# Optimization experiments

Hardware: AMD Instinct MI355X
Metric: run time of the kernel (lower is better)

The kernel has to match this reference:

```python
import jax, jax.numpy as jnp
import numpy as np

H = 16  # n_heads (init kwarg)


def pos_enc(length, dim):
    # torch PositionalEncoding: pe[:,0::2]=sin, pe[:,1::2]=cos
    pos = jnp.arange(length, dtype=jnp.float32)[:, None]
    div = jnp.exp(jnp.arange(0, dim, 2, dtype=jnp.float32) * (-np.log(10000.0) / dim))
    ang = pos * div  # [L, dim/2]
    return jnp.stack([jnp.sin(ang), jnp.cos(ang)], axis=-1).reshape(length, dim)


def torch_ln(x, a, b, eps=1e-6):
    # custom LayerNorm: a*(x-mean)/(std+eps)+b with unbiased std (torch default)
    mean = x.mean(-1, keepdims=True)
    n = x.shape[-1]
    var = ((x - mean) ** 2).sum(-1, keepdims=True) / (n - 1)
    return a * (x - mean) / (jnp.sqrt(var) + eps) + b


def setup_inputs() -> dict:
    key = jax.random.key(0)
    ks = jax.random.split(key, 16)
    B, Lq, Lk, qd, kd, hid, mid = 8, 512, 1024, 768, 768, 1024, 4096
    s = 0.02  # weight init scale
    w = lambda k, shape: jax.random.normal(k, shape, jnp.float32) * s
    return dict(
        q=jax.random.normal(ks[0], (B, Lq, qd), jnp.float32),
        k=jax.random.normal(ks[1], (B, Lk, kd), jnp.float32),
        Wq=w(ks[2], (qd, hid)), bq=jnp.zeros(hid, jnp.float32),
        Wk=w(ks[3], (kd, hid)), bk=jnp.zeros(hid, jnp.float32),
        Wv=w(ks[4], (kd, hid)), bv=jnp.zeros(hid, jnp.float32),
        Wv0=w(ks[5], (kd, hid)), bv0=jnp.zeros(hid, jnp.float32),
        Wq0=w(ks[6], (qd, hid)), bq0=jnp.zeros(hid, jnp.float32),
        nq_a=jnp.ones(hid, jnp.float32), nq_b=jnp.zeros(hid, jnp.float32),
        nx_a=jnp.ones(hid, jnp.float32), nx_b=jnp.zeros(hid, jnp.float32),
        W1=w(ks[7], (hid, mid)), b1=jnp.zeros(mid, jnp.float32),
        W2=w(ks[8], (mid, hid)), b2=jnp.zeros(hid, jnp.float32),
        ns_a=jnp.ones(hid, jnp.float32), ns_b=jnp.zeros(hid, jnp.float32),
    )


def reference(q, k, Wq, bq, Wk, bk, Wv, bv, Wv0, bv0, Wq0, bq0,
              nq_a, nq_b, nx_a, nx_b, W1, b1, W2, b2, ns_a, ns_b):
    # FocalAtt(mode='CA').forward(q, k, PE='qk', SF=True, outmode='atted_bilinear')
    B, Lq, qd = q.shape
    Lk, kd = k.shape[1], k.shape[2]
    hid = Wq.shape[1]
    dh = hid // H
    q0 = q
    qp = q + pos_enc(Lq, qd)  # PosEnc_q (dropout=0)
    kp = k + pos_enc(Lk, kd)  # PosEnc_k
    # AttM: manual multi-head scores
    qh = (qp @ Wq + bq).reshape(B, Lq, H, dh).transpose(0, 2, 1, 3)  # bhqd
    kh = (kp @ Wk + bk).reshape(B, Lk, H, dh).transpose(0, 2, 1, 3)  # bhkd
    scores = jnp.einsum('bhqd,bhkd->bhqk', qh, kh) / jnp.sqrt(jnp.float32(dh))
    att = jax.nn.softmax(scores, axis=-1)  # SF=True
    q0p = q0 @ Wq0 + bq0  # [B, Lq, hid]
    # 'atted' branch
    v1 = (kp @ Wv + bv).reshape(B, Lk, H, dh).transpose(0, 2, 1, 3)
    atted = jnp.einsum('bhqk,bhkd->bhqd', att, v1)
    atted = atted.transpose(0, 2, 1, 3).reshape(B, Lq, hid)
    atted = torch_ln(q0p + atted, nq_a, nq_b)
    # 'bilinear' branch: einsum('bhvk,bhvq,bhqk->bhk')
    q0h = q0p.reshape(B, Lq, H, dh).transpose(0, 2, 1, 3)  # bhvd, v=Lq
    v0 = (kp @ Wv0 + bv0).reshape(B, Lk, H, dh).transpose(0, 2, 1, 3)  # bhqd, q=Lk
    x = jnp.einsum('bhvd,bhvq,bhqd->bhd', q0h, att, v0).reshape(B, hid)
    x = torch_ln(x, nx_a, nx_b)
    # attention output: relu over scores, mean over heads
    att_out = jax.nn.relu(scores).sum(axis=1) / jnp.float32(H)  # [B, Lq, Lk]
    # SorCA: FFN + residual + LayerNorm
    ff = jax.nn.relu(atted @ W1 + b1) @ W2 + b2
    qq = torch_ln(atted + ff, ns_a, ns_b)
    # FocalAtt returns (feature, q, k, attention, attidx_q, attidx_k); drop Nones
    return (x, qq, kp, att_out)
```

## Files before the change

kernel.cpp:

```cpp
#include <hip/hip_runtime.h>


typedef unsigned short bfr;
using short8 = __attribute__((ext_vector_type(8))) short;
using f32x4  = __attribute__((ext_vector_type(4))) float;

__device__ __forceinline__ float b2f(bfr s) {
  return __uint_as_float(((unsigned int)s) << 16);
}
__device__ __forceinline__ bfr f2b(float f) {
  unsigned int u = __float_as_uint(f);
  u += 0x7fffu + ((u >> 16) & 1u);
  return (bfr)(u >> 16);
}

struct __align__(8) us4 { bfr x, y, z, w; };

__device__ __forceinline__ float4 load4f(const float* p) { return *(const float4*)p; }
__device__ __forceinline__ float4 load4f(const bfr* p) {
  us4 u = *(const us4*)p;
  return make_float4(b2f(u.x), b2f(u.y), b2f(u.z), b2f(u.w));
}
__device__ __forceinline__ void store4(float* p, float a, float b, float c, float d) {
  *(float4*)p = make_float4(a, b, c, d);
}
__device__ __forceinline__ void store4(bfr* p, float a, float b, float c, float d) {
  us4 v; v.x = f2b(a); v.y = f2b(b); v.z = f2b(c); v.w = f2b(d);
  *(us4*)p = v;
}

__device__ __forceinline__ void gll16(const bfr* g, bfr* l) {
  __builtin_amdgcn_global_load_lds(
      (const __attribute__((address_space(1))) unsigned int*)g,
      (__attribute__((address_space(3))) unsigned int*)l, 16, 0, 0);
}

__device__ __forceinline__ int swz_off(int row, int chunk) {
  return row * 64 + ((chunk ^ (row & 7)) * 8);
}

__device__ __forceinline__ float pe_val(int l, int d) {
  float ang = (float)l * expf((float)(d & ~1) * (-9.210340371976184f / 768.0f));
  return (d & 1) ? cosf(ang) : sinf(ang);
}

__global__ __launch_bounds__(256) void posenc_k(const float* __restrict__ in,
                                                float* __restrict__ outf,
                                                bfr* __restrict__ outb, int total) {
  int idx = blockIdx.x * 256 + threadIdx.x;
  if (idx >= total) return;
  float v = in[idx] + pe_val((idx / 768) % 1024, idx % 768);
  outf[idx] = v;
  outb[idx] = f2b(v);
}

__global__ __launch_bounds__(256) void posenc_q_all(const float* __restrict__ in,
                                                    bfr* __restrict__ out,
                                                    bfr* __restrict__ outraw,
                                                    int total) {
  int idx = blockIdx.x * 256 + threadIdx.x;
  if (idx >= total) return;
  float v = in[idx];
  out[idx] = f2b(v + pe_val((idx / 768) % 512, idx % 768));
  outraw[idx] = f2b(v);
}

__global__ __launch_bounds__(256) void transpose_w(const float* __restrict__ src,
                                                   bfr* __restrict__ dst,
                                                   int rows, int cols, int ld,
                                                   int mode) {
  __shared__ float t[32][33];
  const int bc = blockIdx.x * 32, br = blockIdx.y * 32;
  const int tx = threadIdx.x & 31, ty = threadIdx.x >> 5;
#pragma unroll
  for (int i = 0; i < 4; i++)
    t[ty + i * 8][tx] = src[(size_t)(br + ty + i * 8) * ld + bc + tx];
  __syncthreads();
#pragma unroll
  for (int i = 0; i < 4; i++) {
    int c = bc + ty + i * 8;
    int r = (mode == 0) ? c : ((c >> 6) * 128 + (c & 63) + (mode == 2 ? 64 : 0));
    dst[(size_t)r * rows + br + tx] = f2b(t[tx][ty + i * 8]);
  }
}

template <typename TC>
__device__ __forceinline__ void mgemm_body64(const bfr* __restrict__ A,
                                             const bfr* __restrict__ BT,
                                             const float* __restrict__ bias,
                                             TC* __restrict__ C,
                                             int K, int ldc, int relu, int accum,
                                             int m0, int n0,
                                             bfr* __restrict__ As,
                                             bfr* __restrict__ Bs) {
  const int tid = threadIdx.x;
  const int lane = tid & 63, w = tid >> 6;
  const int wm = (w & 1) * 64, wn = (w >> 1) * 32;
  const int grow = lane >> 3;
  const int gkc = ((lane & 7) ^ (lane >> 3)) * 8;
  const int fr = lane & 15, fcg = lane >> 4;
  const int NT = K >> 6;
  f32x4 acc[4][2];
#pragma unroll
  for (int i = 0; i < 4; i++)
#pragma unroll
    for (int j = 0; j < 2; j++) acc[i][j] = (f32x4){0.f, 0.f, 0.f, 0.f};

  auto issue = [&](int t, int buf) {
    const int k0 = t << 6;
    const bfr* Ag = A + (size_t)(m0 + w * 32 + grow) * K + k0 + gkc;
#pragma unroll
    for (int i = 0; i < 4; i++)
      gll16(Ag + (size_t)(i * 8) * K, As + buf * 8192 + (w * 32 + i * 8) * 64);
    const bfr* Bg = BT + (size_t)(n0 + w * 16 + grow) * K + k0 + gkc;
#pragma unroll
    for (int i = 0; i < 2; i++)
      gll16(Bg + (size_t)(i * 8) * K, Bs + buf * 4096 + (w * 16 + i * 8) * 64);
  };

  issue(0, 0);
  asm volatile("s_waitcnt vmcnt(0)" ::: "memory");
  __builtin_amdgcn_s_barrier();
  __builtin_amdgcn_sched_barrier(0);
  int cur = 0;
  for (int t = 0; t < NT; ++t) {
    const bool more = (t + 1 < NT);
    if (more) issue(t + 1, cur ^ 1);
    __builtin_amdgcn_s_setprio(1);
#pragma unroll
    for (int ks = 0; ks < 2; ks++) {
      short8 af[4], bf4[2];
#pragma unroll
      for (int i = 0; i < 4; i++)
        af[i] = *(const short8*)(As + cur * 8192 + swz_off(wm + i * 16 + fr, ks * 4 + fcg));
#pragma unroll
      for (int j = 0; j < 2; j++)
        bf4[j] = *(const short8*)(Bs + cur * 4096 + swz_off(wn + j * 16 + fr, ks * 4 + fcg));
#pragma unroll
      for (int i = 0; i < 4; i++)
#pragma unroll
        for (int j = 0; j < 2; j++)
          acc[i][j] = __builtin_amdgcn_mfma_f32_16x16x32_bf16(af[i], bf4[j], acc[i][j], 0, 0, 0);
    }
    __builtin_amdgcn_s_setprio(0);
    if (more) {
      asm volatile("s_waitcnt vmcnt(0)" ::: "memory");
      __builtin_amdgcn_s_barrier();
      __builtin_amdgcn_sched_barrier(0);
      cur ^= 1;
    }
  }
  const int col0 = n0 + wn + fr;
  const int row0 = m0 + wm + (lane >> 4) * 4;
  float bsv[2];
#pragma unroll
  for (int j = 0; j < 2; j++) bsv[j] = bias ? bias[col0 + j * 16] : 0.f;
#pragma unroll
  for (int i = 0; i < 4; i++) {
#pragma unroll
    for (int j = 0; j < 2; j++) {
      const int col = col0 + j * 16;
#pragma unroll
      for (int r = 0; r < 4; r++) {
        const int row = row0 + i * 16 + r;
        float v = acc[i][j][r] + bsv[j];
        if (relu) v = fmaxf(v, 0.f);
        size_t idx = (size_t)row * ldc + col;
        if constexpr (sizeof(TC) == 2) {
          C[idx] = f2b(v);
        } else {
          if (accum) C[idx] += v; else C[idx] = v;
        }
      }
    }
  }
}

template <typename TC>
__global__ __launch_bounds__(256) void mgemm64(const bfr* __restrict__ A,
                                               const bfr* __restrict__ BT,
                                               const float* __restrict__ bias,
                                               TC* __restrict__ C,
                                               int K, int ldc, int relu, int accum) {
  __shared__ bfr As[2][8192];
  __shared__ bfr Bs[2][4096];
  const int nwg = gridDim.x * gridDim.y;
  const int bid = blockIdx.y * gridDim.x + blockIdx.x;
  const int q8 = nwg >> 3, r8 = nwg & 7;
  const int xcd = bid & 7, off = bid >> 3;
  const int swz = (xcd < r8 ? xcd * (q8 + 1) : r8 * (q8 + 1) + (xcd - r8) * q8) + off;
  const int n0 = (swz % gridDim.x) * 64, m0 = (swz / gridDim.x) * 128;
  mgemm_body64<TC>(A, BT, bias, C, K, ldc, relu, accum, m0, n0,
                   &As[0][0], &Bs[0][0]);
}

__global__ __launch_bounds__(256) void kv_gemm2(const bfr* __restrict__ kp0,
                                                const bfr* __restrict__ kp1,
                                                const bfr* __restrict__ WkT,
                                                const float* __restrict__ bk,
                                                bfr* __restrict__ kh0,
                                                bfr* __restrict__ kh1,
                                                const bfr* __restrict__ WTvv,
                                                bfr* __restrict__ vT0,
                                                bfr* __restrict__ vT1) {
  __shared__ bfr As[2][8192];
  __shared__ bfr Bs[2][4096];
  const int swz = (blockIdx.x & 7) * 96 + (blockIdx.x >> 3);
  if (swz < 128) {
    mgemm_body64<bfr>(kp0, WkT, bk, kh0, 768, 1024, 0, 0,
                      (swz >> 4) * 128, (swz & 15) * 64, &As[0][0], &Bs[0][0]);
  } else if (swz < 256) {
    const int s = swz - 128;
    mgemm_body64<bfr>(kp1, WkT, bk, kh1, 768, 1024, 0, 0,
                      (s >> 4) * 128, (s & 15) * 64, &As[0][0], &Bs[0][0]);
  } else if (swz < 512) {
    const int s = swz - 256;
    mgemm_body64<bfr>(WTvv, kp0, nullptr, vT0, 768, 1024, 0, 0,
                      (s >> 4) * 128, (s & 15) * 64, &As[0][0], &Bs[0][0]);
  } else {
    const int s = swz - 512;
    mgemm_body64<bfr>(WTvv, kp1, nullptr, vT1, 768, 1024, 0, 0,
                      (s >> 4) * 128, (s & 15) * 64, &As[0][0], &Bs[0][0]);
  }
}

__global__ __launch_bounds__(256) void proj_gemm(const bfr* __restrict__ q16,
                                                 const bfr* __restrict__ Wq0T,
                                                 const float* __restrict__ bq0,
                                                 bfr* __restrict__ q0p,
                                                 const bfr* __restrict__ qp_all,
                                                 const bfr* __restrict__ WqT,
                                                 const float* __restrict__ bq,
                                                 bfr* __restrict__ qh) {
  __shared__ bfr As[2][8192];
  __shared__ bfr Bs[2][4096];
  const int swz = (blockIdx.x & 7) * 128 + (blockIdx.x >> 3);
  if (swz < 512) {
    mgemm_body64<bfr>(q16, Wq0T, bq0, q0p, 768, 1024, 0, 0,
                      (swz >> 4) * 128, (swz & 15) * 64, &As[0][0], &Bs[0][0]);
  } else {
    const int s = swz - 512;
    mgemm_body64<bfr>(qp_all, WqT, bq, qh, 768, 1024, 0, 0,
                      (s >> 4) * 128, (s & 15) * 64, &As[0][0], &Bs[0][0]);
  }
}

__global__ __launch_bounds__(256) void score_mfma(const bfr* __restrict__ qh,
                                                  const bfr* __restrict__ kh,
                                                  bfr* __restrict__ sc) {
  __shared__ __align__(16) bfr Qs[128][72];
  __shared__ __align__(16) bfr Ks[128][72];
  const int h = blockIdx.z, q0 = blockIdx.y * 128, k0 = blockIdx.x * 128;
  const int tid = threadIdx.x, lane = tid & 63;
  const int wm = ((tid >> 6) & 1) * 64, wn = (tid >> 7) * 64;
  const int fr = lane & 15, fc = (lane >> 4) * 8;
  {
    const int r = tid >> 1, c = (tid & 1) * 32;
    const bfr* qsrc = qh + (size_t)(q0 + r) * 1024 + h * 64 + c;
    const bfr* ksrc = kh + (size_t)(k0 + r) * 1024 + h * 64 + c;
#pragma unroll
    for (int i = 0; i < 4; i++) {
      *(short8*)&Qs[r][c + i * 8] = *(const short8*)(qsrc + i * 8);
      *(short8*)&Ks[r][c + i * 8] = *(const short8*)(ksrc + i * 8);
    }
  }
  __syncthreads();
  f32x4 acc[4][4];
#pragma unroll
  for (int i = 0; i < 4; i++)
#pragma unroll
    for (int j = 0; j < 4; j++) acc[i][j] = (f32x4){0.f, 0.f, 0.f, 0.f};
  __builtin_amdgcn_s_setprio(1);
#pragma unroll
  for (int ks = 0; ks < 2; ks++) {
    short8 af[4], bf[4];
#pragma unroll
    for (int t = 0; t < 4; t++) af[t] = *(const short8*)&Qs[wm + t * 16 + fr][ks * 32 + fc];
#pragma unroll
    for (int t = 0; t < 4; t++) bf[t] = *(const short8*)&Ks[wn + t * 16 + fr][ks * 32 + fc];
#pragma unroll
    for (int i = 0; i < 4; i++)
#pragma unroll
      for (int j = 0; j < 4; j++)
        acc[i][j] = __builtin_amdgcn_mfma_f32_16x16x32_bf16(af[i], bf[j], acc[i][j], 0, 0, 0);
  }
  __builtin_amdgcn_s_setprio(0);
  const int col0 = k0 + wn + fr;
  const int row0 = q0 + wm + (lane >> 4) * 4;
#pragma unroll
  for (int i = 0; i < 4; i++)
#pragma unroll
    for (int j = 0; j < 4; j++)
#pragma unroll
      for (int r = 0; r < 4; r++)
        sc[((size_t)h * 512 + row0 + i * 16 + r) * 1024 + col0 + j * 16] =
            f2b(acc[i][j][r] * 0.125f);
}

__global__ __launch_bounds__(256) void smax_ao(bfr* __restrict__ sc,
                                               float* __restrict__ ao) {
  __shared__ float part[4][1024];
  const int q = blockIdx.x;
  const int tid = threadIdx.x, lane = tid & 63, w = tid >> 6;
  float aos[16];
#pragma unroll
  for (int i = 0; i < 16; i++) aos[i] = 0.f;
#pragma unroll
  for (int i = 0; i < 4; i++) {
    const int h = w * 4 + i;
    bfr* row = sc + ((size_t)h * 512 + q) * 1024 + lane * 16;
    us4 raw[4];
    float v[16];
#pragma unroll
    for (int j = 0; j < 4; j++) raw[j] = ((const us4*)row)[j];
#pragma unroll
    for (int j = 0; j < 4; j++) {
      v[j * 4 + 0] = b2f(raw[j].x); v[j * 4 + 1] = b2f(raw[j].y);
      v[j * 4 + 2] = b2f(raw[j].z); v[j * 4 + 3] = b2f(raw[j].w);
    }
    float m = v[0];
#pragma unroll
    for (int j = 1; j < 16; j++) m = fmaxf(m, v[j]);
#pragma unroll
    for (int j = 0; j < 16; j++) aos[j] += fmaxf(v[j], 0.f);
    for (int o = 32; o; o >>= 1) m = fmaxf(m, __shfl_xor(m, o, 64));
    float s = 0.f;
#pragma unroll
    for (int j = 0; j < 16; j++) { v[j] = expf(v[j] - m); s += v[j]; }
    for (int o = 32; o; o >>= 1) s += __shfl_xor(s, o, 64);
    const float inv = 1.0f / s;
#pragma unroll
    for (int j = 0; j < 4; j++) {
      raw[j].x = f2b(v[j * 4 + 0] * inv); raw[j].y = f2b(v[j * 4 + 1] * inv);
      raw[j].z = f2b(v[j * 4 + 2] * inv); raw[j].w = f2b(v[j * 4 + 3] * inv);
      ((us4*)row)[j] = raw[j];
    }
  }
#pragma unroll
  for (int j = 0; j < 4; j++)
    *(float4*)&part[w][lane * 16 + j * 4] =
        make_float4(aos[j * 4], aos[j * 4 + 1], aos[j * 4 + 2], aos[j * 4 + 3]);
  __syncthreads();
  const int k4 = tid * 4;
  float4 a0 = *(const float4*)&part[0][k4];
  float4 a1 = *(const float4*)&part[1][k4];
  float4 a2 = *(const float4*)&part[2][k4];
  float4 a3 = *(const float4*)&part[3][k4];
  store4(ao + (size_t)q * 1024 + k4,
         (a0.x + a1.x + a2.x + a3.x) * 0.0625f, (a0.y + a1.y + a2.y + a3.y) * 0.0625f,
         (a0.z + a1.z + a2.z + a3.z) * 0.0625f, (a0.w + a1.w + a2.w + a3.w) * 0.0625f);
}

__global__ __launch_bounds__(256) void attv3(const bfr* __restrict__ att,
                                             const bfr* __restrict__ vT,
                                             const float* __restrict__ bv,
                                             const float* __restrict__ bv0,
                                             bfr* __restrict__ atp,
                                             bfr* __restrict__ u) {
  __shared__ bfr As[2][16 * 64];
  __shared__ bfr Bs[2][128 * 64];
  const int h = blockIdx.y, q0 = blockIdx.x * 16;
  const int tid = threadIdx.x, lane = tid & 63, w = tid >> 6;
  const int fr = lane & 15, fcg = lane >> 4;
  const int wn = w * 32;
  const bfr* attb = att + ((size_t)h * 512 + q0) * 1024;
  const bfr* vb = vT + (size_t)h * 128 * 1024;
  const int grow = lane >> 3;
  const int gkc = ((lane & 7) ^ (lane >> 3)) * 8;
  f32x4 acc[2];
#pragma unroll
  for (int j = 0; j < 2; j++) acc[j] = (f32x4){0.f, 0.f, 0.f, 0.f};

  auto issue = [&](int t, int buf) {
    const int k0 = t << 6;
    if (w < 2)
      gll16(attb + (size_t)(w * 8 + grow) * 1024 + k0 + gkc, &As[buf][(w * 8) * 64]);
#pragma unroll
    for (int i = 0; i < 4; i++)
      gll16(vb + (size_t)(wn + i * 8 + grow) * 1024 + k0 + gkc,
            &Bs[buf][(wn + i * 8) * 64]);
  };

  issue(0, 0);
  asm volatile("s_waitcnt vmcnt(0)" ::: "memory");
  __builtin_amdgcn_s_barrier();
  __builtin_amdgcn_sched_barrier(0);
  int cur = 0;
  for (int t = 0; t < 16; ++t) {
    const bool more = (t + 1 < 16);
    if (more) issue(t + 1, cur ^ 1);
    __builtin_amdgcn_s_setprio(1);
#pragma unroll
    for (int ks = 0; ks < 2; ks++) {
      short8 af = *(const short8*)&As[cur][swz_off(fr, ks * 4 + fcg)];
#pragma unroll
      for (int j = 0; j < 2; j++) {
        short8 bf = *(const short8*)&Bs[cur][swz_off(wn + j * 16 + fr, ks * 4 + fcg)];
        acc[j] = __builtin_amdgcn_mfma_f32_16x16x32_bf16(af, bf, acc[j], 0, 0, 0);
      }
    }
    __builtin_amdgcn_s_setprio(0);
    if (more) {
      asm volatile("s_waitcnt vmcnt(0)" ::: "memory");
      __builtin_amdgcn_s_barrier();
      __builtin_amdgcn_sched_barrier(0);
      cur ^= 1;
    }
  }
  const int row0 = q0 + (lane >> 4) * 4;
  bfr* o = (w < 2) ? atp : u;
  const float* bias = (w < 2) ? bv : bv0;
  const int dbase = wn & 63;
#pragma unroll
  for (int j = 0; j < 2; j++) {
    const int cm = dbase + j * 16 + fr;
    const float bb = bias[h * 64 + cm];
#pragma unroll
    for (int r = 0; r < 4; r++)
      o[(size_t)(row0 + r) * 1024 + h * 64 + cm] = f2b(acc[j][r] + bb);
  }
}

__global__ __launch_bounds__(256) void xpre2(const bfr* __restrict__ q0p0,
                                             const bfr* __restrict__ u0,
                                             float* __restrict__ xpre0) {
  const int c = blockIdx.x * 256 + threadIdx.x;
  const int r0 = blockIdx.y * 64;
  const int j = blockIdx.z;
  const bfr* qp = q0p0 + (size_t)j * 524288 + (size_t)r0 * 1024 + c;
  const bfr* up = u0 + (size_t)j * 1048576 + (size_t)r0 * 1024 + c;
  float s = 0.f;
#pragma unroll 8
  for (int r = 0; r < 64; r++)
    s = fmaf(b2f(qp[(size_t)r * 1024]), b2f(up[(size_t)r * 1024]), s);
  atomicAdd(&xpre0[j * 1024 + c], s);
}

template <typename OT>
__device__ __forceinline__ void ln_body(float4 v, const float* ga, const float* be,
                                        OT* outp, int tid, float* sm) {
  float s = v.x + v.y + v.z + v.w;
  for (int o = 32; o; o >>= 1) s += __shfl_down(s, o, 64);
  if ((tid & 63) == 0) sm[tid >> 6] = s;
  __syncthreads();
  s = sm[0] + sm[1] + sm[2] + sm[3];
  float mean = s * (1.0f / 1024.0f);
  float d0 = v.x - mean, d1 = v.y - mean, d2 = v.z - mean, d3 = v.w - mean;
  float q = d0 * d0 + d1 * d1 + d2 * d2 + d3 * d3;
  __syncthreads();
  for (int o = 32; o; o >>= 1) q += __shfl_down(q, o, 64);
  if ((tid & 63) == 0) sm[tid >> 6] = q;
  __syncthreads();
  q = sm[0] + sm[1] + sm[2] + sm[3];
  float rs = 1.0f / (sqrtf(q * (1.0f / 1023.0f)) + 1e-6f);
  float4 g = *(const float4*)(ga + tid * 4);
  float4 bb = *(const float4*)(be + tid * 4);
  store4(outp, g.x * d0 * rs + bb.x, g.y * d1 * rs + bb.y,
         g.z * d2 * rs + bb.z, g.w * d3 * rs + bb.w);
}

template <typename TX, typename TY, typename OT>
__global__ __launch_bounds__(256) void ln_kernel(const TX* __restrict__ X,
                                                 const TY* __restrict__ Y,
                                                 const float* __restrict__ ga,
                                                 const float* __restrict__ be,
                                                 OT* __restrict__ out) {
  __shared__ float sm[4];
  const size_t row = blockIdx.x;
  const int tid = threadIdx.x;
  float4 v = load4f(X + row * 1024 + tid * 4);
  if (Y) {
    float4 w = load4f(Y + row * 1024 + tid * 4);
    v.x += w.x; v.y += w.y; v.z += w.z; v.w += w.w;
  }
  ln_body(v, ga, be, out + row * 1024 + tid * 4, tid, sm);
}

__global__ __launch_bounds__(256) void ln2_kernel(const bfr* __restrict__ q0p0,
                                                  const bfr* __restrict__ atp0,
                                                  const float* __restrict__ ga,
                                                  const float* __restrict__ be,
                                                  bfr* __restrict__ atl0) {
  __shared__ float sm[4];
  const int row = blockIdx.x;
  const int b = row >> 9, r = row & 511;
  const int tid = threadIdx.x;
  float4 v = load4f(q0p0 + (size_t)b * 524288 + (size_t)r * 1024 + tid * 4);
  float4 w = load4f(atp0 + (size_t)b * 1048576 + (size_t)r * 1024 + tid * 4);
  v.x += w.x; v.y += w.y; v.z += w.z; v.w += w.w;
  ln_body(v, ga, be, atl0 + (size_t)b * 524288 + (size_t)r * 1024 + tid * 4, tid, sm);
}

extern "C" void kernel_launch(void* const* d_in, const int* in_sizes, int n_in,
                              void* d_out, int out_size, void* d_ws, size_t ws_size,
                              hipStream_t stream) {
  (void)in_sizes; (void)n_in; (void)out_size; (void)ws_size;
  const float* q   = (const float*)d_in[0];
  const float* k   = (const float*)d_in[1];
  const float* Wq  = (const float*)d_in[2];
  const float* bq  = (const float*)d_in[3];
  const float* Wk  = (const float*)d_in[4];
  const float* bk  = (const float*)d_in[5];
  const float* Wv  = (const float*)d_in[6];
  const float* bv  = (const float*)d_in[7];
  const float* Wv0 = (const float*)d_in[8];
  const float* bv0 = (const float*)d_in[9];
  const float* Wq0 = (const float*)d_in[10];
  const float* bq0 = (const float*)d_in[11];
  const float* nqa = (const float*)d_in[12];
  const float* nqb = (const float*)d_in[13];
  const float* nxa = (const float*)d_in[14];
  const float* nxb = (const float*)d_in[15];
  const float* W1  = (const float*)d_in[16];
  const float* b1  = (const float*)d_in[17];
  const float* W2  = (const float*)d_in[18];
  const float* b2  = (const float*)d_in[19];
  const float* nsa = (const float*)d_in[20];
  const float* nsb = (const float*)d_in[21];

  float* out = (float*)d_out;
  float* x_out  = out;
  float* qq_out = out + 8192;
  float* kp_out = out + 4202496;
  float* ao_out = out + 10493952;
  bfr* kp16 = (bfr*)qq_out;
  bfr* vT1  = kp16 + 6291456;

  char* base = (char*)d_ws;
  bfr* q0p   = (bfr*)(base + 0);
  bfr* qh    = (bfr*)(base + 8388608);
  bfr* atl   = (bfr*)(base + 16777216);
  bfr* WqT   = (bfr*)(base + 25165824);
  bfr* Wq0T  = (bfr*)(base + 26738688);
  bfr* WTkv  = (bfr*)(base + 28311552);
  float* xpre = (float*)(base + 33030144);
  char* S = base + 33062912;
  bfr* sc    = (bfr*)(S + 0);
  bfr* kh0   = (bfr*)(S + 16777216);
  bfr* kh1   = (bfr*)(S + 18874368);
  bfr* vT0   = (bfr*)(S + 20971520);
  bfr* atp0  = (bfr*)(S + 16777216);
  bfr* ub0   = (bfr*)(S + 17825792);
  bfr* atp1  = (bfr*)(S + 18874368);
  bfr* ub1   = (bfr*)(S + 19922944);
  bfr* qp_all = (bfr*)(S + 0);
  bfr* q16    = (bfr*)(S + 6291456);
  bfr* W1Tn  = (bfr*)(S + 0);
  bfr* W2Tn  = (bfr*)(S + 4194304);
  bfr* ff1n  = (bfr*)(S + 8388608);
  float* ff2a = (float*)(base + 0);

  posenc_k<<<24576, 256, 0, stream>>>(k, kp_out, kp16, 6291456);
  posenc_q_all<<<12288, 256, 0, stream>>>(q, qp_all, q16, 3145728);
  transpose_w<<<dim3(32, 24), 256, 0, stream>>>(Wq, WqT, 768, 1024, 1024, 0);
  transpose_w<<<dim3(32, 24), 256, 0, stream>>>(Wq0, Wq0T, 768, 1024, 1024, 0);
  transpose_w<<<dim3(32, 24), 256, 0, stream>>>(Wk, WTkv, 768, 1024, 1024, 0);
  transpose_w<<<dim3(32, 24), 256, 0, stream>>>(Wv, WTkv + 786432, 768, 1024, 1024, 1);
  transpose_w<<<dim3(32, 24), 256, 0, stream>>>(Wv0, WTkv + 786432, 768, 1024, 1024, 2);

  proj_gemm<<<1024, 256, 0, stream>>>(q16, Wq0T, bq0, q0p, qp_all, WqT, bq, qh);
  hipMemsetAsync(xpre, 0, 32768, stream);

  for (int p = 0; p < 4; p++) {
    const int b0 = 2 * p;
    kv_gemm2<<<768, 256, 0, stream>>>(kp16 + (size_t)b0 * 786432,
                                      kp16 + (size_t)(b0 + 1) * 786432,
                                      WTkv, bk, kh0, kh1,
                                      WTkv + 786432, vT0, vT1);
    for (int j = 0; j < 2; j++) {
      const int b = b0 + j;
      bfr* kh = j ? kh1 : kh0;
      bfr* vT = j ? vT1 : vT0;
      bfr* atpb = j ? atp1 : atp0;
      bfr* ub = j ? ub1 : ub0;
      score_mfma<<<dim3(8, 4, 16), 256, 0, stream>>>(qh + (size_t)b * 524288, kh, sc);
      smax_ao<<<512, 256, 0, stream>>>(sc, ao_out + (size_t)b * 524288);
      attv3<<<dim3(32, 16), 256, 0, stream>>>(sc, vT, bv, bv0, atpb, ub);
    }
    xpre2<<<dim3(4, 8, 2), 256, 0, stream>>>(q0p + (size_t)b0 * 524288, ub0,
                                             xpre + b0 * 1024);
    ln2_kernel<<<1024, 256, 0, stream>>>(q0p + (size_t)b0 * 524288, atp0,
                                         nqa, nqb, atl + (size_t)b0 * 524288);
  }

  ln_kernel<float, float, float><<<8, 256, 0, stream>>>(xpre, (const float*)nullptr,
                                                        nxa, nxb, x_out);

  for (int nc = 0; nc < 2; nc++) {
    transpose_w<<<dim3(64, 32), 256, 0, stream>>>(W1 + nc * 2048, W1Tn,
                                                  1024, 2048, 4096, 0);
    transpose_w<<<dim3(32, 64), 256, 0, stream>>>(W2 + (size_t)nc * 2048 * 1024, W2Tn,
                                                  2048, 1024, 1024, 0);
    mgemm64<bfr><<<dim3(32, 32), 256, 0, stream>>>(
        atl, W1Tn, b1 + nc * 2048, ff1n, 1024, 2048, 1, 0);
    mgemm64<float><<<dim3(16, 32), 256, 0, stream>>>(
        ff1n, W2Tn, nc == 0 ? b2 : nullptr, ff2a, 2048, 1024, 0, nc);
  }
  ln_kernel<bfr, float, float><<<4096, 256, 0, stream>>>(atl, ff2a, nsa, nsb, qq_out);
}
```

Measured before the change: 719.5 us.

## Fuse softmax into attention-value kernel and split relu head-mean into own kernel

Moves the row softmax from the separate smax_ao kernel into the attention-times-V kernel. Each block now reads its 16 score rows, normalizes them in registers, and keeps the probabilities in LDS instead of writing them back to global memory and streaming them in again. The relu head-mean output becomes a simple elementwise kernel that reads all 16 heads. This drops one bf16 write and one read of the full score tensor per batch. In exchange, the attention kernel uses much more LDS and registers (64 floats per thread), and its MFMA loop cannot start until the softmax prologue finishes.

After: 713.4 us. Within noise of the previous version (-0.9%).

```diff
diff --git a/kernel.cpp b/kernel.cpp
--- a/kernel.cpp
+++ b/kernel.cpp
@@ -297,102 +297,90 @@
             f2b(acc[i][j][r] * 0.125f);
 }
 
-__global__ __launch_bounds__(256) void smax_ao(bfr* __restrict__ sc,
+__global__ __launch_bounds__(256) void attout8(const bfr* __restrict__ sc,
                                                float* __restrict__ ao) {
-  __shared__ float part[4][1024];
-  const int q = blockIdx.x;
-  const int tid = threadIdx.x, lane = tid & 63, w = tid >> 6;
-  float aos[16];
-#pragma unroll
-  for (int i = 0; i < 16; i++) aos[i] = 0.f;
-#pragma unroll
-  for (int i = 0; i < 4; i++) {
-    const int h = w * 4 + i;
-    bfr* row = sc + ((size_t)h * 512 + q) * 1024 + lane * 16;
-    us4 raw[4];
-    float v[16];
-#pragma unroll
-    for (int j = 0; j < 4; j++) raw[j] = ((const us4*)row)[j];
-#pragma unroll
-    for (int j = 0; j < 4; j++) {
-      v[j * 4 + 0] = b2f(raw[j].x); v[j * 4 + 1] = b2f(raw[j].y);
-      v[j * 4 + 2] = b2f(raw[j].z); v[j * 4 + 3] = b2f(raw[j].w);
-    }
-    float m = v[0];
-#pragma unroll
-    for (int j = 1; j < 16; j++) m = fmaxf(m, v[j]);
-#pragma unroll
-    for (int j = 0; j < 16; j++) aos[j] += fmaxf(v[j], 0.f);
-    for (int o = 32; o; o >>= 1) m = fmaxf(m, __shfl_xor(m, o, 64));
-    float s = 0.f;
-#pragma unroll
-    for (int j = 0; j < 16; j++) { v[j] = expf(v[j] - m); s += v[j]; }
-    for (int o = 32; o; o >>= 1) s += __shfl_xor(s, o, 64);
-    const float inv = 1.0f / s;
-#pragma unroll
-    for (int j = 0; j < 4; j++) {
-      raw[j].x = f2b(v[j * 4 + 0] * inv); raw[j].y = f2b(v[j * 4 + 1] * inv);
-      raw[j].z = f2b(v[j * 4 + 2] * inv); raw[j].w = f2b(v[j * 4 + 3] * inv);
-      ((us4*)row)[j] = raw[j];
-    }
-  }
-#pragma unroll
-  for (int j = 0; j < 4; j++)
-    *(float4*)&part[w][lane * 16 + j * 4] =
-        make_float4(aos[j * 4], aos[j * 4 + 1], aos[j * 4 + 2], aos[j * 4 + 3]);
-  __syncthreads();
-  const int k4 = tid * 4;
-  float4 a0 = *(const float4*)&part[0][k4];
-  float4 a1 = *(const float4*)&part[1][k4];
-  float4 a2 = *(const float4*)&part[2][k4];
-  float4 a3 = *(const float4*)&part[3][k4];
-  store4(ao + (size_t)q * 1024 + k4,
-         (a0.x + a1.x + a2.x + a3.x) * 0.0625f, (a0.y + a1.y + a2.y + a3.y) * 0.0625f,
-         (a0.z + a1.z + a2.z + a3.z) * 0.0625f, (a0.w + a1.w + a2.w + a3.w) * 0.0625f);
-}
-
-__global__ __launch_bounds__(256) void attv3(const bfr* __restrict__ att,
+  const int i8 = (blockIdx.x * 256 + threadIdx.x) * 8;
+  float s[8] = {};
+#pragma unroll
+  for (int h = 0; h < 16; h++) {
+    short8 r = *(const short8*)(sc + (size_t)h * 524288 + i8);
+#pragma unroll
+    for (int e = 0; e < 8; e++) s[e] += fmaxf(b2f((bfr)r[e]), 0.f);
+  }
+  store4(ao + i8, s[0] * 0.0625f, s[1] * 0.0625f, s[2] * 0.0625f, s[3] * 0.0625f);
+  store4(ao + i8 + 4, s[4] * 0.0625f, s[5] * 0.0625f, s[6] * 0.0625f, s[7] * 0.0625f);
+}
+
+__global__ __launch_bounds__(256) void attv4(const bfr* __restrict__ sc,
                                              const bfr* __restrict__ vT,
                                              const float* __restrict__ bv,
                                              const float* __restrict__ bv0,
                                              bfr* __restrict__ atp,
                                              bfr* __restrict__ u) {
-  __shared__ bfr As[2][16 * 64];
+  __shared__ bfr attL[16][1032];
   __shared__ bfr Bs[2][128 * 64];
   const int h = blockIdx.y, q0 = blockIdx.x * 16;
   const int tid = threadIdx.x, lane = tid & 63, w = tid >> 6;
   const int fr = lane & 15, fcg = lane >> 4;
   const int wn = w * 32;
-  const bfr* attb = att + ((size_t)h * 512 + q0) * 1024;
   const bfr* vb = vT + (size_t)h * 128 * 1024;
   const int grow = lane >> 3;
   const int gkc = ((lane & 7) ^ (lane >> 3)) * 8;
-  f32x4 acc[2];
-#pragma unroll
-  for (int j = 0; j < 2; j++) acc[j] = (f32x4){0.f, 0.f, 0.f, 0.f};
-
-  auto issue = [&](int t, int buf) {
+
+  auto issueV = [&](int t, int buf) {
     const int k0 = t << 6;
-    if (w < 2)
-      gll16(attb + (size_t)(w * 8 + grow) * 1024 + k0 + gkc, &As[buf][(w * 8) * 64]);
 #pragma unroll
     for (int i = 0; i < 4; i++)
       gll16(vb + (size_t)(wn + i * 8 + grow) * 1024 + k0 + gkc,
             &Bs[buf][(wn + i * 8) * 64]);
   };
 
-  issue(0, 0);
+  issueV(0, 0);
+
+  const int row = tid >> 4, seg = tid & 15;
+  const bfr* srow = sc + ((size_t)h * 512 + q0 + row) * 1024;
+  short8 raw[8];
+#pragma unroll
+  for (int j = 0; j < 8; j++)
+    raw[j] = *(const short8*)(srow + j * 128 + seg * 8);
+  float v[64];
+#pragma unroll
+  for (int j = 0; j < 8; j++)
+#pragma unroll
+    for (int e = 0; e < 8; e++)
+      v[j * 8 + e] = b2f((bfr)raw[j][e]);
+  float m = v[0];
+#pragma unroll
+  for (int i = 1; i < 64; i++) m = fmaxf(m, v[i]);
+#pragma unroll
+  for (int o = 1; o < 16; o <<= 1) m = fmaxf(m, __shfl_xor(m, o, 64));
+  float s = 0.f;
+#pragma unroll
+  for (int i = 0; i < 64; i++) { v[i] = expf(v[i] - m); s += v[i]; }
+#pragma unroll
+  for (int o = 1; o < 16; o <<= 1) s += __shfl_xor(s, o, 64);
+  const float inv = 1.0f / s;
+#pragma unroll
+  for (int j = 0; j < 8; j++) {
+    short8 pw;
+#pragma unroll
+    for (int e = 0; e < 8; e++) pw[e] = (short)f2b(v[j * 8 + e] * inv);
+    *(short8*)&attL[row][j * 128 + seg * 8] = pw;
+  }
   asm volatile("s_waitcnt vmcnt(0)" ::: "memory");
-  __builtin_amdgcn_s_barrier();
-  __builtin_amdgcn_sched_barrier(0);
+  __syncthreads();
+
+  f32x4 acc[2];
+#pragma unroll
+  for (int j = 0; j < 2; j++) acc[j] = (f32x4){0.f, 0.f, 0.f, 0.f};
   int cur = 0;
   for (int t = 0; t < 16; ++t) {
     const bool more = (t + 1 < 16);
-    if (more) issue(t + 1, cur ^ 1);
+    if (more) issueV(t + 1, cur ^ 1);
     __builtin_amdgcn_s_setprio(1);
 #pragma unroll
     for (int ks = 0; ks < 2; ks++) {
-      short8 af = *(const short8*)&As[cur][swz_off(fr, ks * 4 + fcg)];
+      short8 af = *(const short8*)&attL[fr][(t << 6) + ks * 32 + fcg * 8];
 #pragma unroll
       for (int j = 0; j < 2; j++) {
         short8 bf = *(const short8*)&Bs[cur][swz_off(wn + j * 16 + fr, ks * 4 + fcg)];
@@ -574,8 +562,8 @@
       bfr* atpb = j ? atp1 : atp0;
       bfr* ub = j ? ub1 : ub0;
       score_mfma<<<dim3(8, 4, 16), 256, 0, stream>>>(qh + (size_t)b * 524288, kh, sc);
-      smax_ao<<<512, 256, 0, stream>>>(sc, ao_out + (size_t)b * 524288);
-      attv3<<<dim3(32, 16), 256, 0, stream>>>(sc, vT, bv, bv0, atpb, ub);
+      attout8<<<256, 256, 0, stream>>>(sc, ao_out + (size_t)b * 524288);
+      attv4<<<dim3(32, 16), 256, 0, stream>>>(sc, vT, bv, bv0, atpb, ub);
     }
     xpre2<<<dim3(4, 8, 2), 256, 0, stream>>>(q0p + (size_t)b0 * 524288, ub0,
                                              xpre + b0 * 1024);
```
